# Optimization experiments

Measured on AMD Instinct MI355X. Metric: run time of the kernel, lower is better.

Reference implementation:

```python
import jax, jax.numpy as jnp
import numpy as np
import math

V, T, E, N = 32000, 128, 64, 1024
SIGMA_MIN, SIGMA_MAX, C = 0.1, 10.0, 2.0


def setup_inputs() -> dict:
    key = jax.random.key(0)
    k1, k2, k3, k4, k5 = jax.random.split(key, 5)
    return {
        "x": jax.random.normal(k1, (T, N), dtype=jnp.float32),
        "mu": jax.random.normal(k2, (V, E), dtype=jnp.float32),
        "log_sigma": jax.random.normal(k3, (V, E), dtype=jnp.float32),
        "mu_c": jax.random.normal(k4, (T, E), dtype=jnp.float32),
        "log_sigma_c": jax.random.normal(k5, (T, E), dtype=jnp.float32),
        "t": 0,
    }


def reference(x, mu, log_sigma, mu_c, log_sigma_c, t):
    # parameter clamping done in-place in the torch forward
    bound = math.sqrt(C)
    mu = jnp.clip(mu, -bound, bound)
    mu_c = jnp.clip(mu_c, -bound, bound)
    log_sigma = jnp.clip(log_sigma, math.log(SIGMA_MIN), math.log(SIGMA_MAX))
    log_sigma_c = jnp.clip(log_sigma_c, math.log(SIGMA_MIN), math.log(SIGMA_MAX))

    sigma = jnp.exp(log_sigma)        # [V, E]
    sigma_c = jnp.exp(log_sigma_c)    # [T, E]

    # pairwise Gaussian expected-likelihood energy, vectorized over topics
    s = sigma[:, None, :] + sigma_c[None, :, :]            # [V, T, E]
    det_fac = jnp.sum(jnp.log(s), axis=-1)                 # [V, T]
    diff = mu[:, None, :] - mu_c[None, :, :]               # [V, T, E]
    diff_mu = jnp.sum(diff * diff / s, axis=-1)            # [V, T]
    emb_dim = mu.shape[-1]
    log_el = -0.5 * (det_fac + diff_mu + emb_dim * math.log(2.0 * math.pi))

    # per-topic softmax over the vocab axis
    w = jax.nn.softmax(log_el, axis=0)                     # [V, T]

    return w @ x.reshape(-1, x.shape[-1])                  # [V, N]
```

## Files before the change

### kernel.cpp

```cpp
#include <hip/hip_runtime.h>
#include <math.h>

#define VV 32000
#define TT 128
#define EE 64
#define NN 1024
#define NPART 500

static constexpr float BOUND    = 1.41421356237309515f;
static constexpr float LOG_SMIN = -2.30258509299404568f;
static constexpr float LOG_SMAX =  2.30258509299404568f;
static constexpr float LN2      =  0.69314718055994531f;
static constexpr float E_LOG2PI =  64.0f * 1.83787706640934548f;

typedef __attribute__((ext_vector_type(2)))  float f32x2;
typedef __attribute__((ext_vector_type(8)))  short short8;
typedef __attribute__((ext_vector_type(16))) float float16;

static __device__ inline unsigned short f2bf(float f) {
    union { float f; unsigned u; } v; v.f = f;
    unsigned r = v.u + 0x7FFFu + ((v.u >> 16) & 1u);
    return (unsigned short)(r >> 16);
}

__global__ __launch_bounds__(256) void logits_kernel(const float* __restrict__ mu,
                                                     const float* __restrict__ log_sigma,
                                                     const float* __restrict__ mu_c,
                                                     const float* __restrict__ log_sigma_c,
                                                     float* __restrict__ logitsT,
                                                     float* __restrict__ pm,
                                                     float* __restrict__ pl) {
    __shared__ float smem[16384];
    float (*stage_s)[65] = (float(*)[65])smem;
    float (*stage_m)[65] = (float(*)[65])(smem + 4160);
    const int tid = threadIdx.x;
    const int v0 = blockIdx.x * 64;

    for (int k = tid; k < 64 * EE; k += 256) {
        int vi = k >> 6, e = k & 63;
        float ls = log_sigma[(v0 + vi) * EE + e];
        ls = fminf(fmaxf(ls, LOG_SMIN), LOG_SMAX);
        stage_s[e][vi] = __expf(ls);
        float m = mu[(v0 + vi) * EE + e];
        stage_m[e][vi] = fminf(fmaxf(m, -BOUND), BOUND);
    }
    __syncthreads();

    const int lane = tid & 63;
    const int wv   = tid >> 6;

    f32x2 sv[EE / 2], mv[EE / 2];
#pragma unroll
    for (int e = 0; e < EE / 2; e++) {
        sv[e] = f32x2{stage_s[2 * e][lane], stage_s[2 * e + 1][lane]};
        mv[e] = f32x2{stage_m[2 * e][lane], stage_m[2 * e + 1][lane]};
    }
    __syncthreads();

    float* scl = smem;
    float* mcl = smem + 8192;
    for (int i = tid; i < TT * EE; i += 256) {
        float ls = log_sigma_c[i];
        ls = fminf(fmaxf(ls, LOG_SMIN), LOG_SMAX);
        scl[i] = __expf(ls);
        float m = mu_c[i];
        mcl[i] = fminf(fmaxf(m, -BOUND), BOUND);
    }
    __syncthreads();

    for (int t = wv; t < TT; t += 4) {
        const f32x2* __restrict__ srow = (const f32x2*)(scl + t * EE);
        const f32x2* __restrict__ mrow = (const f32x2*)(mcl + t * EE);
        float acc_l2 = 0.0f;
        f32x2 q = {0.0f, 0.0f};
#pragma unroll
        for (int g = 0; g < 4; g++) {
            f32x2 p = {1.0f, 1.0f};
#pragma unroll
            for (int h = 0; h < 8; h++) {
                int e2 = g * 8 + h;
                f32x2 s = sv[e2] + srow[e2];
                p *= s;
                f32x2 d = mv[e2] - mrow[e2];
                f32x2 r;
                r.x = __builtin_amdgcn_rcpf(s.x);
                r.y = __builtin_amdgcn_rcpf(s.y);
                q += d * d * r;
            }
            acc_l2 += __log2f(p.x * p.y);
        }
        float logit = -0.5f * (acc_l2 * LN2 + (q.x + q.y) + E_LOG2PI);
        logitsT[t * VV + v0 + lane] = logit;

        float m = logit;
#pragma unroll
        for (int off = 1; off < 64; off <<= 1) m = fmaxf(m, __shfl_xor(m, off));
        float s = __expf(logit - m);
#pragma unroll
        for (int off = 1; off < 64; off <<= 1) s += __shfl_xor(s, off);
        if (lane == 0) {
            int j = t * NPART + blockIdx.x;
            pm[j] = m;
            pl[j] = s;
        }
    }
}

__global__ __launch_bounds__(256) void merge_xpose(const float* __restrict__ pm,
                                                   const float* __restrict__ pl,
                                                   const float* __restrict__ x,
                                                   float* __restrict__ stats,
                                                   unsigned short* __restrict__ xT) {
    const int tid = threadIdx.x;
    __shared__ float red[8];
    if (blockIdx.x < TT) {
        const int t = blockIdx.x;
        float m = -3.4e38f;
        for (int j = tid; j < NPART; j += 256) m = fmaxf(m, pm[t * NPART + j]);
#pragma unroll
        for (int off = 1; off < 64; off <<= 1) m = fmaxf(m, __shfl_xor(m, off));
        if ((tid & 63) == 0) red[tid >> 6] = m;
        __syncthreads();
        m = fmaxf(fmaxf(red[0], red[1]), fmaxf(red[2], red[3]));

        float l = 0.0f;
        for (int j = tid; j < NPART; j += 256)
            l += pl[t * NPART + j] * __expf(pm[t * NPART + j] - m);
#pragma unroll
        for (int off = 1; off < 64; off <<= 1) l += __shfl_xor(l, off);
        if ((tid & 63) == 0) red[4 + (tid >> 6)] = l;
        __syncthreads();
        if (tid == 0) {
            float tot = red[4] + red[5] + red[6] + red[7];
            stats[t] = m;
            stats[TT + t] = 1.0f / tot;
        }
    } else {
        const int b = blockIdx.x - TT;
        const int n = b * 128 + (tid & 127);
        const int th = tid >> 7;
        const float* __restrict__ xp = x + n;
#pragma unroll
        for (int i = 0; i < 64; i += 2) {
            int t = th * 64 + i;
            float x0 = xp[(size_t)t * NN];
            float x1 = xp[(size_t)(t + 1) * NN];
            *(unsigned*)&xT[n * TT + t] = (unsigned)f2bf(x0) | ((unsigned)f2bf(x1) << 16);
        }
    }
}

__global__ __launch_bounds__(256) void make_w(const float* __restrict__ logitsT,
                                              const float* __restrict__ stats,
                                              unsigned short* __restrict__ w) {
    __shared__ __attribute__((aligned(16))) unsigned short wl[64][136];
    __shared__ float sl[256];
    const int tid = threadIdx.x;
    const int v0 = blockIdx.x * 64;

    sl[tid] = stats[tid];
    __syncthreads();

    {
        const int v = tid & 63;
        const int tg = tid >> 6;
        const float* __restrict__ lp = logitsT + v0 + v;
#pragma unroll
        for (int i = 0; i < 32; i += 2) {
            int t = tg * 32 + i;
            float lg0 = lp[(size_t)t * VV];
            float lg1 = lp[(size_t)(t + 1) * VV];
            float w0 = __expf(lg0 - sl[t])     * sl[TT + t];
            float w1 = __expf(lg1 - sl[t + 1]) * sl[TT + t + 1];
            *(unsigned*)&wl[v][t] = (unsigned)f2bf(w0) | ((unsigned)f2bf(w1) << 16);
        }
    }
    __syncthreads();

    {
        const int v = tid >> 2;
        const int seg = (tid & 3) * 32;
#pragma unroll
        for (int j = 0; j < 4; j++) {
            uint4 d = *(const uint4*)&wl[v][seg + j * 8];
            *(uint4*)&w[(size_t)(v0 + v) * TT + seg + j * 8] = d;
        }
    }
}

__global__ __launch_bounds__(256) void wx_mfma(const unsigned short* __restrict__ w,
                                               const unsigned short* __restrict__ xT,
                                               float* __restrict__ out) {
    const int tid = threadIdx.x;
    const int v0 = blockIdx.x * 64;
    const int n0 = blockIdx.y * 128;
    const int lane = tid & 63;
    const int wv   = tid >> 6;
    const int vh   = (wv & 1) * 32;
    const int nh   = (wv >> 1) * 64;
    const int r32  = lane & 31;
    const int koff = (lane >> 5) * 8;

    const unsigned short* __restrict__ ap  = w  + (size_t)(v0 + vh + r32) * TT + koff;
    const unsigned short* __restrict__ bp0 = xT + (size_t)(n0 + nh + r32) * TT + koff;
    const unsigned short* __restrict__ bp1 = bp0 + 32 * TT;

    float16 acc0 = {0,0,0,0,0,0,0,0,0,0,0,0,0,0,0,0};
    float16 acc1 = {0,0,0,0,0,0,0,0,0,0,0,0,0,0,0,0};
#pragma unroll
    for (int kb = 0; kb < 8; kb++) {
        short8 a  = *(const short8*)(ap  + kb * 16);
        short8 b0 = *(const short8*)(bp0 + kb * 16);
        short8 b1 = *(const short8*)(bp1 + kb * 16);
        acc0 = __builtin_amdgcn_mfma_f32_32x32x16_bf16(a, b0, acc0, 0, 0, 0);
        acc1 = __builtin_amdgcn_mfma_f32_32x32x16_bf16(a, b1, acc1, 0, 0, 0);
    }

    const int col = lane & 31;
    const int rbase = 4 * (lane >> 5);
#pragma unroll
    for (int r = 0; r < 16; r++) {
        int row = (r & 3) + 8 * (r >> 2) + rbase;
        float* dst = out + (size_t)(v0 + vh + row) * NN + n0 + nh + col;
        dst[0]  = acc0[r];
        dst[32] = acc1[r];
    }
}

extern "C" void kernel_launch(void* const* d_in, const int* in_sizes, int n_in,
                              void* d_out, int out_size, void* d_ws, size_t ws_size,
                              hipStream_t stream) {
    const float* x           = (const float*)d_in[0];
    const float* mu          = (const float*)d_in[1];
    const float* log_sigma   = (const float*)d_in[2];
    const float* mu_c        = (const float*)d_in[3];
    const float* log_sigma_c = (const float*)d_in[4];
    float* out = (float*)d_out;

    float* ws      = (float*)d_ws;
    float* logitsT = ws;
    float* pm      = logitsT + (size_t)TT * VV;
    float* pl      = pm + (size_t)TT * NPART;
    float* stats   = pl + (size_t)TT * NPART;
    unsigned short* w_bf16 = (unsigned short*)(stats + 2 * TT);
    unsigned short* xT     = w_bf16 + (size_t)VV * TT;

    logits_kernel<<<VV / 64, 256, 0, stream>>>(mu, log_sigma, mu_c, log_sigma_c,
                                               logitsT, pm, pl);
    merge_xpose<<<TT + NN / 128, 256, 0, stream>>>(pm, pl, x, stats, xT);
    make_w<<<VV / 64, 256, 0, stream>>>(logitsT, stats, w_bf16);
    wx_mfma<<<dim3(VV / 64, NN / 128), 256, 0, stream>>>(w_bf16, xT, out);
}
```

Baseline: 270.4 us.

## Split logits work across embedding slices and topic halves with precomputed context

Moves the clamp and exp of the context parameters into a small separate kernel so the logits blocks no longer recompute them into shared memory. The logits kernel now runs on a 2D grid over vocab and topic halves. Each wave takes a 16-wide slice of the embedding, the per-topic partial energies are reduced through shared memory, and the context rows are read with wave-uniform addresses. This is meant to raise parallelism and cut register and LDS pressure, at the cost of an extra launch, extra barriers, and duplicated loads of mu and log_sigma across the two topic halves.

New measurement: 250.9 us. -7.2%, faster.

```diff
diff --git a/kernel.cpp b/kernel.cpp
--- a/kernel.cpp
+++ b/kernel.cpp
@@ -23,86 +23,97 @@
     return (unsigned short)(r >> 16);
 }
 
+__global__ __launch_bounds__(256) void prep_ctx(const float* __restrict__ mu_c,
+                                                const float* __restrict__ log_sigma_c,
+                                                float* __restrict__ sc,
+                                                float* __restrict__ mc) {
+    int i = blockIdx.x * 256 + threadIdx.x;
+    if (i < TT * EE) {
+        float ls = log_sigma_c[i];
+        ls = fminf(fmaxf(ls, LOG_SMIN), LOG_SMAX);
+        sc[i] = __expf(ls);
+        float m = mu_c[i];
+        mc[i] = fminf(fmaxf(m, -BOUND), BOUND);
+    }
+}
+
 __global__ __launch_bounds__(256) void logits_kernel(const float* __restrict__ mu,
                                                      const float* __restrict__ log_sigma,
-                                                     const float* __restrict__ mu_c,
-                                                     const float* __restrict__ log_sigma_c,
+                                                     const float* __restrict__ sc,
+                                                     const float* __restrict__ mc,
                                                      float* __restrict__ logitsT,
                                                      float* __restrict__ pm,
                                                      float* __restrict__ pl) {
-    __shared__ float smem[16384];
-    float (*stage_s)[65] = (float(*)[65])smem;
-    float (*stage_m)[65] = (float(*)[65])(smem + 4160);
-    const int tid = threadIdx.x;
-    const int v0 = blockIdx.x * 64;
-
-    for (int k = tid; k < 64 * EE; k += 256) {
-        int vi = k >> 6, e = k & 63;
-        float ls = log_sigma[(v0 + vi) * EE + e];
-        ls = fminf(fmaxf(ls, LOG_SMIN), LOG_SMAX);
-        stage_s[e][vi] = __expf(ls);
-        float m = mu[(v0 + vi) * EE + e];
-        stage_m[e][vi] = fminf(fmaxf(m, -BOUND), BOUND);
-    }
-    __syncthreads();
-
+    __shared__ float part[8][4][64];
+    const int tid  = threadIdx.x;
     const int lane = tid & 63;
     const int wv   = tid >> 6;
-
-    f32x2 sv[EE / 2], mv[EE / 2];
-#pragma unroll
-    for (int e = 0; e < EE / 2; e++) {
-        sv[e] = f32x2{stage_s[2 * e][lane], stage_s[2 * e + 1][lane]};
-        mv[e] = f32x2{stage_m[2 * e][lane], stage_m[2 * e + 1][lane]};
-    }
-    __syncthreads();
-
-    float* scl = smem;
-    float* mcl = smem + 8192;
-    for (int i = tid; i < TT * EE; i += 256) {
-        float ls = log_sigma_c[i];
-        ls = fminf(fmaxf(ls, LOG_SMIN), LOG_SMAX);
-        scl[i] = __expf(ls);
-        float m = mu_c[i];
-        mcl[i] = fminf(fmaxf(m, -BOUND), BOUND);
-    }
-    __syncthreads();
-
-    for (int t = wv; t < TT; t += 4) {
-        const f32x2* __restrict__ srow = (const f32x2*)(scl + t * EE);
-        const f32x2* __restrict__ mrow = (const f32x2*)(mcl + t * EE);
-        float acc_l2 = 0.0f;
-        f32x2 q = {0.0f, 0.0f};
-#pragma unroll
-        for (int g = 0; g < 4; g++) {
-            f32x2 p = {1.0f, 1.0f};
-#pragma unroll
-            for (int h = 0; h < 8; h++) {
-                int e2 = g * 8 + h;
-                f32x2 s = sv[e2] + srow[e2];
-                p *= s;
-                f32x2 d = mv[e2] - mrow[e2];
+    const int v0   = blockIdx.x * 64;
+    const int t0   = blockIdx.y * 64;
+    const int e0   = wv * 16;
+    const int e0u  = __builtin_amdgcn_readfirstlane(wv) * 16;
+
+    f32x2 sv[8], mv[8];
+    {
+        const float* __restrict__ lsp = log_sigma + (size_t)(v0 + lane) * EE + e0;
+        const float* __restrict__ mup = mu        + (size_t)(v0 + lane) * EE + e0;
+#pragma unroll
+        for (int j = 0; j < 8; j++) {
+            float a = lsp[2 * j], b = lsp[2 * j + 1];
+            a = fminf(fmaxf(a, LOG_SMIN), LOG_SMAX);
+            b = fminf(fmaxf(b, LOG_SMIN), LOG_SMAX);
+            sv[j] = f32x2{__expf(a), __expf(b)};
+            float c = mup[2 * j], d = mup[2 * j + 1];
+            mv[j] = f32x2{fminf(fmaxf(c, -BOUND), BOUND), fminf(fmaxf(d, -BOUND), BOUND)};
+        }
+    }
+
+    for (int tb = 0; tb < 8; tb++) {
+        f32x2 q[8], p[8];
+#pragma unroll
+        for (int i = 0; i < 8; i++) { q[i] = f32x2{0.f, 0.f}; p[i] = f32x2{1.f, 1.f}; }
+#pragma unroll
+        for (int i = 0; i < 8; i++) {
+            const int t = t0 + tb * 8 + i;
+            const f32x2* __restrict__ srow = (const f32x2*)(sc + t * EE + e0u);
+            const f32x2* __restrict__ mrow = (const f32x2*)(mc + t * EE + e0u);
+#pragma unroll
+            for (int j = 0; j < 8; j++) {
+                f32x2 s = sv[j] + srow[j];
+                p[i] *= s;
+                f32x2 d = mv[j] - mrow[j];
                 f32x2 r;
                 r.x = __builtin_amdgcn_rcpf(s.x);
                 r.y = __builtin_amdgcn_rcpf(s.y);
-                q += d * d * r;
+                q[i] += d * d * r;
             }
-            acc_l2 += __log2f(p.x * p.y);
-        }
-        float logit = -0.5f * (acc_l2 * LN2 + (q.x + q.y) + E_LOG2PI);
-        logitsT[t * VV + v0 + lane] = logit;
-
-        float m = logit;
-#pragma unroll
-        for (int off = 1; off < 64; off <<= 1) m = fmaxf(m, __shfl_xor(m, off));
-        float s = __expf(logit - m);
-#pragma unroll
-        for (int off = 1; off < 64; off <<= 1) s += __shfl_xor(s, off);
-        if (lane == 0) {
-            int j = t * NPART + blockIdx.x;
-            pm[j] = m;
-            pl[j] = s;
-        }
+        }
+#pragma unroll
+        for (int i = 0; i < 8; i++) {
+            float contrib = __log2f(p[i].x * p[i].y) * LN2 + q[i].x + q[i].y;
+            part[i][wv][lane] = contrib;
+        }
+        __syncthreads();
+#pragma unroll
+        for (int k = 0; k < 2; k++) {
+            const int i = wv * 2 + k;
+            const int t = t0 + tb * 8 + i;
+            float sum = part[i][0][lane] + part[i][1][lane] + part[i][2][lane] + part[i][3][lane];
+            float logit = -0.5f * (sum + E_LOG2PI);
+            logitsT[t * VV + v0 + lane] = logit;
+
+            float m = logit;
+#pragma unroll
+            for (int off = 1; off < 64; off <<= 1) m = fmaxf(m, __shfl_xor(m, off));
+            float sx = __expf(logit - m);
+#pragma unroll
+            for (int off = 1; off < 64; off <<= 1) sx += __shfl_xor(sx, off);
+            if (lane == 0) {
+                pm[t * NPART + blockIdx.x] = m;
+                pl[t * NPART + blockIdx.x] = sx;
+            }
+        }
+        __syncthreads();
     }
 }
 
@@ -242,11 +253,14 @@
     float* pm      = logitsT + (size_t)TT * VV;
     float* pl      = pm + (size_t)TT * NPART;
     float* stats   = pl + (size_t)TT * NPART;
-    unsigned short* w_bf16 = (unsigned short*)(stats + 2 * TT);
+    float* sc      = stats + 2 * TT;
+    float* mc      = sc + TT * EE;
+    unsigned short* w_bf16 = (unsigned short*)(mc + TT * EE);
     unsigned short* xT     = w_bf16 + (size_t)VV * TT;
 
-    logits_kernel<<<VV / 64, 256, 0, stream>>>(mu, log_sigma, mu_c, log_sigma_c,
-                                               logitsT, pm, pl);
+    prep_ctx<<<(TT * EE + 255) / 256, 256, 0, stream>>>(mu_c, log_sigma_c, sc, mc);
+    logits_kernel<<<dim3(VV / 64, 2), 256, 0, stream>>>(mu, log_sigma, sc, mc,
+                                                        logitsT, pm, pl);
     merge_xpose<<<TT + NN / 128, 256, 0, stream>>>(pm, pl, x, stats, xT);
     make_w<<<VV / 64, 256, 0, stream>>>(logitsT, stats, w_bf16);
     wx_mfma<<<dim3(VV / 64, NN / 128), 256, 0, stream>>>(w_bf16, xT, out);
```
